# Performance work log

Hardware: AMD Instinct MI355X
Metric: run time of the kernel (lower is better)

Reference implementation:

```python
import jax, jax.numpy as jnp
import numpy as np

DIM = 2                 # spatial dimension (fixed to 2 in the source)
T = 6                   # number_of_time_points
DT = 1.0 / (T - 1)


def _mlp(z, W1, b1, W2, b2, W3, b3):
    # Linear_Tanh(4->10), Linear_Tanh(10->10), Linear(10->3)
    h = jnp.tanh(z @ W1 + b1)
    h = jnp.tanh(h @ W2 + b2)
    return h @ W3 + b3


def _sym_block(o):
    # o[...,3] -> symmetric 2x2 block: off-diag o[...,0], diag exp(o[...,1]), exp(o[...,2])
    off = o[..., 0]
    row0 = jnp.stack([jnp.exp(o[..., 1]), off], axis=-1)
    row1 = jnp.stack([off, jnp.exp(o[..., 2])], axis=-1)
    return jnp.stack([row0, row1], axis=-2)


def _kernel_blocks(x, y, params):
    # x: [b, nx, 2], y: [b, ny, 2] -> pairwise 2x2 kernel blocks [b, nx, ny, 2, 2]
    b, nx, _ = x.shape
    ny = y.shape[1]
    xx = jnp.broadcast_to(x[:, :, None, :], (b, nx, ny, DIM))
    yy = jnp.broadcast_to(y[:, None, :, :], (b, nx, ny, DIM))
    K1 = _sym_block(_mlp(jnp.concatenate([xx, yy], axis=-1), *params))
    K2 = _sym_block(_mlp(jnp.concatenate([yy, xx], axis=-1), *params))
    return 0.5 * (K1 + K2)


def _matvec(K, q):
    # block-matrix vector product: K [b,nx,ny,2,2] @ q [b,ny,2] -> [b,nx,2]
    return jnp.einsum('bxyij,byj->bxi', K, q)


def _forward(q_0, template_points, control_points, W1, b1, W2, b2, W3, b3):
    params = (W1, b1, W2, b2, W3, b3)
    bts = q_0.shape[0]
    p = jnp.broadcast_to(control_points[None], (bts,) + control_points.shape)
    p_t, q_t = [p], [q_0]

    def ham(pp, qq):
        dh_dq = _matvec(_kernel_blocks(pp, pp, params), qq)
        return 0.5 * jnp.sum(qq * dh_dq), dh_dq

    # Hamiltonian shooting: T steps of symplectic-Euler-like integration
    for _ in range(T):
        pc, qc = p_t[-1], q_t[-1]
        (_, dh_dq), dh_dp = jax.value_and_grad(ham, has_aux=True)(pc, qc)
        p_t.append(pc + DT * dh_dq)
        q_t.append(qc - DT * dh_dp)

    # flow the template points along the time-varying velocity field
    x = jnp.broadcast_to(template_points[None], (bts,) + template_points.shape)
    for pc, qc in zip(p_t, q_t):
        x = x + DT * _matvec(_kernel_blocks(x, pc, params), qc)
    return x


def setup_inputs() -> dict:
    key = jax.random.key(0)
    ks = jax.random.split(key, 8)
    bts, ncp, ntpl, H = 16, 64, 2048, 10
    # 8x8 control-point grid over [-2.5, 2.5]^2 (compute_grid with margin 0)
    ax = jnp.linspace(-2.5, 2.5, 8, dtype=jnp.float32)
    gx, gy = jnp.meshgrid(ax, ax, indexing='ij')
    control_points = jnp.stack([gx, gy], axis=-1).reshape(ncp, DIM)
    template_points = jax.random.normal(ks[0], (ntpl, DIM), dtype=jnp.float32)
    q_0 = 0.05 * jax.random.normal(ks[1], (bts, ncp, DIM), dtype=jnp.float32)
    W1 = 0.5 * jax.random.normal(ks[2], (2 * DIM, H), dtype=jnp.float32)
    b1 = jnp.zeros((H,), dtype=jnp.float32)
    W2 = 0.5 * jax.random.normal(ks[3], (H, H), dtype=jnp.float32)
    b2 = jnp.zeros((H,), dtype=jnp.float32)
    W3 = 0.5 * jax.random.normal(ks[4], (H, DIM * (DIM + 1) // 2), dtype=jnp.float32)
    b3 = jnp.zeros((DIM * (DIM + 1) // 2,), dtype=jnp.float32)
    return {'q_0': q_0, 'template_points': template_points, 'control_points': control_points,
            'W1': W1, 'b1': b1, 'W2': W2, 'b2': b2, 'W3': W3, 'b3': b3}


def reference(q_0, template_points, control_points, W1, b1, W2, b2, W3, b3):
    return _forward(q_0, template_points, control_points, W1, b1, W2, b2, W3, b3)
```

## Files before the change

kernel.cpp:

```cpp
#include <hip/hip_runtime.h>
#include <hip/hip_fp16.h>

#define NCP    64
#define BTS    16
#define NTPL   2048
#define TSTEPS 6
#define DTF    0.2f
#define L2E    1.4426950408889634f

__device__ __forceinline__ float fast_rcp(float x) { return __builtin_amdgcn_rcpf(x); }
__device__ __forceinline__ float fexp2(float x)    { return __builtin_amdgcn_exp2f(x); }
__device__ __forceinline__ float fast_tanh(float x) {
    float e = __expf(2.0f * x);
    return 1.0f - 2.0f * fast_rcp(1.0f + e);
}

__device__ __forceinline__ void load_raw_w(
    const float* __restrict__ W1, const float* __restrict__ b1,
    const float* __restrict__ W2, const float* __restrict__ W3,
    int lane, float (&w)[180])
{
    float cA = (lane < 40) ? W1[lane] : (lane < 50 ? b1[lane - 40] : 0.f);
    float cB0 = W2[lane];
    float cB1 = (lane < 36) ? W2[64 + lane] : 0.f;
    float cC  = (lane < 30) ? W3[lane] : 0.f;
#pragma unroll
    for (int t = 0; t < 50; ++t)  w[t] = __shfl(cA, t);
#pragma unroll
    for (int t = 0; t < 64; ++t)  w[50 + t] = __shfl(cB0, t);
#pragma unroll
    for (int t = 0; t < 36; ++t)  w[114 + t] = __shfl(cB1, t);
#pragma unroll
    for (int t = 0; t < 30; ++t)  w[150 + t] = __shfl(cC, t);
}

__device__ __forceinline__ void load_w_h2(const float* __restrict__ wt,
                                          int lane, __half2 (&wh)[180])
{
    float c0 = wt[lane];
    float c1 = wt[64 + lane];
    float c2 = wt[128 + lane];
#pragma unroll
    for (int t = 0; t < 180; ++t) {
        int src = (t < 150) ? t : (t + 10);
        int ch = src >> 6, ix = src & 63;
        float v = (ch == 0) ? c0 : (ch == 1) ? c1 : c2;
        wh[t] = __float2half2_rn(__shfl(v, ix));
    }
}

__device__ __forceinline__ void kblock4_h2(
    const float (&x0)[4], const float (&x1)[4], float p0, float p1,
    const __half2 (&wh)[180], const __half2 (&b2h)[10], const __half2 (&b3h)[3],
    float (&M00)[4], float (&M01)[4], float (&M11)[4])
{
    const __half2 one = __float2half2_rn(1.0f);

    __half2 Z0[4], Z1[4], Z2[4], Z3[4];
#pragma unroll
    for (int m = 0; m < 4; ++m) {
        Z0[m] = __floats2half2_rn(x0[m], p0);
        Z1[m] = __floats2half2_rn(x1[m], p1);
        Z2[m] = __lowhigh2highlow(Z0[m]);
        Z3[m] = __lowhigh2highlow(Z1[m]);
    }

    __half2 r[4][10];
#pragma unroll
    for (int k = 0; k < 10; ++k) {
        __half2 w0 = wh[k], w1 = wh[10 + k], w2 = wh[20 + k], w3 = wh[30 + k];
        __half2 bb = wh[40 + k];
#pragma unroll
        for (int m = 0; m < 4; ++m) {
            __half2 t = __hfma2(Z3[m], w3,
                        __hfma2(Z2[m], w2,
                        __hfma2(Z1[m], w1,
                        __hfma2(Z0[m], w0, bb))));
            r[m][k] = h2rcp(__hadd2(one, h2exp2(t)));
        }
    }

    __half2 u[4][10];
#pragma unroll
    for (int k = 0; k < 10; ++k) {
        __half2 ww = wh[50 + k];
        __half2 bb = b2h[k];
#pragma unroll
        for (int m = 0; m < 4; ++m) u[m][k] = __hfma2(r[m][0], ww, bb);
    }
#pragma unroll
    for (int c = 1; c < 10; ++c) {
#pragma unroll
        for (int k = 0; k < 10; ++k) {
            __half2 ww = wh[50 + c * 10 + k];
#pragma unroll
            for (int m = 0; m < 4; ++m) u[m][k] = __hfma2(r[m][c], ww, u[m][k]);
        }
    }

    __half2 O[4], A[4], B[4];
#pragma unroll
    for (int m = 0; m < 4; ++m) { O[m] = b3h[0]; A[m] = b3h[1]; B[m] = b3h[2]; }
#pragma unroll
    for (int c = 0; c < 10; ++c) {
        __half2 c0 = wh[150 + c], c1 = wh[160 + c], c2 = wh[170 + c];
#pragma unroll
        for (int m = 0; m < 4; ++m) {
            __half2 g = h2rcp(__hadd2(one, h2exp2(u[m][c])));
            O[m] = __hfma2(g, c0, O[m]);
            A[m] = __hfma2(g, c1, A[m]);
            B[m] = __hfma2(g, c2, B[m]);
        }
    }
#pragma unroll
    for (int m = 0; m < 4; ++m) {
        M00[m] = fexp2(__low2float(A[m])) + fexp2(__high2float(A[m]));
        M01[m] = __low2float(O[m]) + __high2float(O[m]);
        M11[m] = fexp2(__low2float(B[m])) + fexp2(__high2float(B[m]));
    }
}

__device__ __forceinline__ void kblock_s0(
    float x0, float x1, float p0, float p1,
    const float (&w)[180], const float (&b2t)[10], const float (&b3t)[3],
    float& M00, float& M01, float& M11)
{
    float ra[10], rb[10];
#pragma unroll
    for (int k = 0; k < 10; ++k) {
        float ta = fmaf(p1, w[30 + k],
                   fmaf(p0, w[20 + k],
                   fmaf(x1, w[10 + k],
                   fmaf(x0, w[k], w[40 + k]))));
        float tb = fmaf(x1, w[30 + k],
                   fmaf(x0, w[20 + k],
                   fmaf(p1, w[10 + k],
                   fmaf(p0, w[k], w[40 + k]))));
        ra[k] = fast_rcp(1.0f + fexp2(ta));
        rb[k] = fast_rcp(1.0f + fexp2(tb));
    }
    float ua[10], ub[10];
#pragma unroll
    for (int k = 0; k < 10; ++k) {
        float bb = b2t[k];
        ua[k] = fmaf(ra[0], w[50 + k], bb);
        ub[k] = fmaf(rb[0], w[50 + k], bb);
    }
#pragma unroll
    for (int c = 1; c < 10; ++c) {
#pragma unroll
        for (int k = 0; k < 10; ++k) {
            float ww = w[50 + c * 10 + k];
            ua[k] = fmaf(ra[c], ww, ua[k]);
            ub[k] = fmaf(rb[c], ww, ub[k]);
        }
    }
    float Oa = b3t[0], Ob = b3t[0];
    float T1a = b3t[1], T1b = b3t[1];
    float T2a = b3t[2], T2b = b3t[2];
#pragma unroll
    for (int c = 0; c < 10; ++c) {
        float r2a = fast_rcp(1.0f + fexp2(ua[c]));
        float r2b = fast_rcp(1.0f + fexp2(ub[c]));
        Oa  = fmaf(r2a, w[150 + c], Oa);   Ob  = fmaf(r2b, w[150 + c], Ob);
        T1a = fmaf(r2a, w[160 + c], T1a);  T1b = fmaf(r2b, w[160 + c], T1b);
        T2a = fmaf(r2a, w[170 + c], T2a);  T2b = fmaf(r2b, w[170 + c], T2b);
    }
    M00 = fexp2(T1a) + fexp2(T1b);
    M01 = Oa + Ob;
    M11 = fexp2(T2a) + fexp2(T2b);
}

__device__ __forceinline__ void shoot_body(
    int batch, int a, int b,
    float pax, float pay, float qax, float qay,
    float pbx, float pby, float qbx, float qby,
    const float (&w)[180],
    const float* __restrict__ b2, const float* __restrict__ b3,
    float* __restrict__ p_out, float* __restrict__ q_out)
{
    float dhq_x = 0.f, dhq_y = 0.f;
    float g_x = 0.f, g_y = 0.f;
    float cross = fmaf(qax, qby, qay * qbx);

#pragma unroll
    for (int e = 0; e < 2; ++e) {
        float z0 = e ? pbx : pax;
        float z1 = e ? pby : pay;
        float z2 = e ? pax : pbx;
        float z3 = e ? pay : pby;

        float h1[10];
#pragma unroll
        for (int k = 0; k < 10; ++k) {
            float u = fmaf(z3, w[30 + k],
                      fmaf(z2, w[20 + k],
                      fmaf(z1, w[10 + k],
                      fmaf(z0, w[k], w[40 + k]))));
            h1[k] = fast_tanh(u);
        }
        float u2[10];
#pragma unroll
        for (int k = 0; k < 10; ++k) u2[k] = b2[k];
#pragma unroll
        for (int c = 0; c < 10; ++c) {
#pragma unroll
            for (int k = 0; k < 10; ++k) u2[k] = fmaf(h1[c], w[50 + c * 10 + k], u2[k]);
        }
        float h2[10];
        float o0 = b3[0], o1 = b3[1], o2 = b3[2];
#pragma unroll
        for (int c = 0; c < 10; ++c) {
            h2[c] = fast_tanh(u2[c]);
            o0 = fmaf(h2[c], w[150 + c * 3 + 0], o0);
            o1 = fmaf(h2[c], w[150 + c * 3 + 1], o1);
            o2 = fmaf(h2[c], w[150 + c * 3 + 2], o2);
        }
        float e1 = __expf(o1), e2 = __expf(o2);

        dhq_x = fmaf(0.5f, fmaf(e1, qbx, o0 * qby), dhq_x);
        dhq_y = fmaf(0.5f, fmaf(o0, qbx, e2 * qby), dhq_y);

        float d0 = cross;
        float d1 = e1 * qax * qbx;
        float d2 = e2 * qay * qby;

        float du2[10];
#pragma unroll
        for (int c = 0; c < 10; ++c) {
            float dh2 = fmaf(w[150 + c * 3 + 0], d0,
                        fmaf(w[150 + c * 3 + 1], d1, w[150 + c * 3 + 2] * d2));
            du2[c] = dh2 * (1.0f - h2[c] * h2[c]);
        }
        float du1[10];
#pragma unroll
        for (int c = 0; c < 10; ++c) {
            float dh1 = 0.f;
#pragma unroll
            for (int k = 0; k < 10; ++k) dh1 = fmaf(w[50 + c * 10 + k], du2[k], dh1);
            du1[c] = dh1 * (1.0f - h1[c] * h1[c]);
        }
        int c0 = e ? 2 : 0;
        float ga = 0.f, gb = 0.f;
#pragma unroll
        for (int k = 0; k < 10; ++k) {
            ga = fmaf(w[(0 + c0) * 10 + k], du1[k], ga);
            gb = fmaf(w[(1 + c0) * 10 + k], du1[k], gb);
        }
        g_x = fmaf(0.5f, ga, g_x);
        g_y = fmaf(0.5f, gb, g_y);
    }

#pragma unroll
    for (int off = 32; off > 0; off >>= 1) {
        dhq_x += __shfl_xor(dhq_x, off);
        dhq_y += __shfl_xor(dhq_y, off);
        g_x   += __shfl_xor(g_x, off);
        g_y   += __shfl_xor(g_y, off);
    }

    if (b == 0) {
        float* pO = p_out + (batch * NCP + a) * 2;
        float* qO = q_out + (batch * NCP + a) * 2;
        pO[0] = fmaf(DTF, dhq_x, pax);
        pO[1] = fmaf(DTF, dhq_y, pay);
        qO[0] = fmaf(-DTF, g_x, qax);
        qO[1] = fmaf(-DTF, g_y, qay);
    }
}

__global__ __launch_bounds__(64, 1)
void shoot0_fused(const float* __restrict__ q0, const float* __restrict__ cp,
                  const float* __restrict__ tpl,
                  const float* __restrict__ W1, const float* __restrict__ b1,
                  const float* __restrict__ W2, const float* __restrict__ b2,
                  const float* __restrict__ W3, const float* __restrict__ b3,
                  float* __restrict__ p_hist, float* __restrict__ q_hist,
                  float* __restrict__ wt, float* __restrict__ out)
{
    int blk = blockIdx.x;
    int lane = threadIdx.x;

    if (blk < BTS * NCP) {
        float w[180];
        load_raw_w(W1, b1, W2, W3, lane, w);
        int batch = blk >> 6;
        int a = blk & (NCP - 1);
        int b = lane;
        float pax = cp[2 * a], pay = cp[2 * a + 1];
        float pbx = cp[2 * b], pby = cp[2 * b + 1];
        float qax = q0[(batch * NCP + a) * 2 + 0], qay = q0[(batch * NCP + a) * 2 + 1];
        float qbx = q0[(batch * NCP + b) * 2 + 0], qby = q0[(batch * NCP + b) * 2 + 1];
        shoot_body(batch, a, b, pax, pay, qax, qay, pbx, pby, qbx, qby,
                   w, b2, b3,
                   p_hist + (size_t)1 * BTS * NCP * 2,
                   q_hist + (size_t)1 * BTS * NCP * 2);
        return;
    }
    if (blk == BTS * NCP) {
        int t = lane;
        if (t < 40) wt[t] = 2.0f * L2E * W1[t];
        if (t < 10) wt[40 + t] = 2.0f * L2E * b1[t];
        for (int i = t; i < 100; i += 64) wt[50 + i] = -4.0f * L2E * W2[i];
        if (t < 10) {
            float s = b2[t];
            for (int c = 0; c < 10; ++c) s += W2[c * 10 + t];
            wt[150 + t] = 2.0f * L2E * s;
            wt[160 + t] = -W3[t * 3 + 0];
            wt[170 + t] = -2.0f * L2E * W3[t * 3 + 1];
            wt[180 + t] = -2.0f * L2E * W3[t * 3 + 2];
        }
        if (t < 3) {
            float s = b3[t];
            for (int c = 0; c < 10; ++c) s += W3[c * 3 + t];
            wt[190 + t] = (t == 0) ? 0.5f * s : fmaf(L2E, s, -1.0f);
        }
        return;
    }

    int i = blk - (BTS * NCP + 1);
    int j = lane;

    float w[180];
    load_raw_w(W1, b1, W2, W3, j, w);

    float b2t[10], b3t[3];
#pragma unroll
    for (int k = 0; k < 10; ++k) {
        float s = b2[k];
#pragma unroll
        for (int c = 0; c < 10; ++c) s += w[50 + c * 10 + k];
        b2t[k] = 2.0f * L2E * s;
    }
#pragma unroll
    for (int t = 0; t < 3; ++t) {
        float s = b3[t];
#pragma unroll
        for (int c = 0; c < 10; ++c) s += w[150 + c * 3 + t];
        b3t[t] = (t == 0) ? 0.5f * s : fmaf(L2E, s, -1.0f);
    }
#pragma unroll
    for (int t = 0; t < 50; ++t) w[t] *= 2.0f * L2E;
#pragma unroll
    for (int t = 50; t < 150; ++t) w[t] *= -4.0f * L2E;
    {
        float c0a[10], c1a[10], c2a[10];
#pragma unroll
        for (int k = 0; k < 10; ++k) {
            c0a[k] = -w[150 + 3 * k];
            c1a[k] = -2.0f * L2E * w[151 + 3 * k];
            c2a[k] = -2.0f * L2E * w[152 + 3 * k];
        }
#pragma unroll
        for (int k = 0; k < 10; ++k) {
            w[150 + k] = c0a[k];
            w[160 + k] = c1a[k];
            w[170 + k] = c2a[k];
        }
    }

    float x0 = tpl[2 * i], x1 = tpl[2 * i + 1];
    float p0 = cp[2 * j],  p1 = cp[2 * j + 1];

    float M00, M01, M11;
    kblock_s0(x0, x1, p0, p1, w, b2t, b3t, M00, M01, M11);

    const float2* __restrict__ q = (const float2*)q0;
#pragma unroll
    for (int bt = 0; bt < BTS; ++bt) {
        float2 qq = q[bt * NCP + j];
        float vx = fmaf(M00, qq.x, M01 * qq.y);
        float vy = fmaf(M01, qq.x, M11 * qq.y);
#pragma unroll
        for (int off = 32; off > 0; off >>= 1) {
            vx += __shfl_xor(vx, off);
            vy += __shfl_xor(vy, off);
        }
        if (j == 0) {
            out[((size_t)bt * NTPL + i) * 2 + 0] = fmaf(DTF, vx, x0);
            out[((size_t)bt * NTPL + i) * 2 + 1] = fmaf(DTF, vy, x1);
        }
    }
}

__global__ __launch_bounds__(64, 1)
void shoot_step(const float* __restrict__ p_in, const float* __restrict__ q_in,
                float* __restrict__ p_out, float* __restrict__ q_out,
                const float* __restrict__ W1, const float* __restrict__ b1,
                const float* __restrict__ W2, const float* __restrict__ b2,
                const float* __restrict__ W3, const float* __restrict__ b3)
{
    int blk = blockIdx.x;
    int batch = blk >> 6;
    int a = blk & (NCP - 1);
    int b = threadIdx.x;

    float w[180];
    load_raw_w(W1, b1, W2, W3, b, w);

    const float* pB = p_in + batch * NCP * 2;
    const float* qB = q_in + batch * NCP * 2;
    float pax = pB[a * 2 + 0], pay = pB[a * 2 + 1];
    float qax = qB[a * 2 + 0], qay = qB[a * 2 + 1];
    float pbx = pB[b * 2 + 0], pby = pB[b * 2 + 1];
    float qbx = qB[b * 2 + 0], qby = qB[b * 2 + 1];

    shoot_body(batch, a, b, pax, pay, qax, qay, pbx, pby, qbx, qby,
               w, b2, b3, p_out, q_out);
}

__global__ __launch_bounds__(256, 1)
void flow_rest(const float* __restrict__ p_hist, const float* __restrict__ q_hist,
               float* __restrict__ out, const float* __restrict__ wt)
{
    int wid = blockIdx.x * 4 + (threadIdx.x >> 6);
    int j = threadIdx.x & 63;
    int u0 = wid * 4;
    int batch = u0 >> 11;
    int i0 = u0 & (NTPL - 1);

    __half2 wh[180];
    load_w_h2(wt, j, wh);
    __half2 b2h[10], b3h[3];
#pragma unroll
    for (int k = 0; k < 10; ++k) b2h[k] = __float2half2_rn(wt[150 + k]);
#pragma unroll
    for (int t = 0; t < 3; ++t)  b3h[t] = __float2half2_rn(wt[190 + t]);

    const float2* __restrict__ ph = (const float2*)p_hist;
    const float2* __restrict__ qh = (const float2*)q_hist;

    size_t ob = ((size_t)batch * NTPL + i0) * 2;
    float x0[4], x1[4];
#pragma unroll
    for (int m = 0; m < 4; ++m) {
        x0[m] = out[ob + 2 * m];
        x1[m] = out[ob + 2 * m + 1];
    }

#pragma unroll
    for (int s = 0; s < TSTEPS; ++s) {
        int idx = ((s + 1) * BTS + batch) * NCP + j;
        float2 P = ph[idx];
        float2 Q = qh[idx];
        float M00[4], M01[4], M11[4];
        kblock4_h2(x0, x1, P.x, P.y, wh, b2h, b3h, M00, M01, M11);
        float vx[4], vy[4];
#pragma unroll
        for (int m = 0; m < 4; ++m) {
            vx[m] = fmaf(M00[m], Q.x, M01[m] * Q.y);
            vy[m] = fmaf(M01[m], Q.x, M11[m] * Q.y);
        }
#pragma unroll
        for (int off = 32; off > 0; off >>= 1) {
#pragma unroll
            for (int m = 0; m < 4; ++m) {
                vx[m] += __shfl_xor(vx[m], off);
                vy[m] += __shfl_xor(vy[m], off);
            }
        }
#pragma unroll
        for (int m = 0; m < 4; ++m) {
            x0[m] = fmaf(DTF, vx[m], x0[m]);
            x1[m] = fmaf(DTF, vy[m], x1[m]);
        }
    }

    if (j == 0) {
#pragma unroll
        for (int m = 0; m < 4; ++m) {
            out[ob + 2 * m]     = x0[m];
            out[ob + 2 * m + 1] = x1[m];
        }
    }
}

extern "C" void kernel_launch(void* const* d_in, const int* in_sizes, int n_in,
                              void* d_out, int out_size, void* d_ws, size_t ws_size,
                              hipStream_t stream)
{
    const float* q0  = (const float*)d_in[0];
    const float* tpl = (const float*)d_in[1];
    const float* cp  = (const float*)d_in[2];
    const float* W1  = (const float*)d_in[3];
    const float* b1  = (const float*)d_in[4];
    const float* W2  = (const float*)d_in[5];
    const float* b2  = (const float*)d_in[6];
    const float* W3  = (const float*)d_in[7];
    const float* b3  = (const float*)d_in[8];
    float* out = (float*)d_out;

    float* ws = (float*)d_ws;
    const int slab = BTS * NCP * 2;
    float* p_hist = ws;
    float* q_hist = ws + (size_t)7 * slab;
    float* wt     = ws + (size_t)14 * slab;

    shoot0_fused<<<BTS * NCP + 1 + NTPL, 64, 0, stream>>>(
        q0, cp, tpl, W1, b1, W2, b2, W3, b3, p_hist, q_hist, wt, out);

    for (int s = 1; s < TSTEPS; ++s) {
        shoot_step<<<BTS * NCP, 64, 0, stream>>>(
            p_hist + (size_t)s * slab, q_hist + (size_t)s * slab,
            p_hist + (size_t)(s + 1) * slab, q_hist + (size_t)(s + 1) * slab,
            W1, b1, W2, b2, W3, b3);
    }

    flow_rest<<<BTS * NTPL / 16, 256, 0, stream>>>(p_hist, q_hist, out, wt);
}
```

Baseline: 273.9 us.

## Fuse each template flow step into the matching shooting step launch

Replaces the single final flow kernel, which looped over all six time steps, with a combined kernel launched once per shooting step. Each launch runs both the next shooting step and the template-point flow update for the current step, plus a final flow-only launch. The aim is to overlap the small, low-occupancy shooting work with the flow work so the GPU stays busier. In exchange, flow blocks shrink from 256 to 64 threads and the template positions are re-read and re-written in global memory at every step, and weights are reloaded each launch.

New measurement: 329.5 us. 20.3% more time.

```diff
diff --git a/kernel.cpp b/kernel.cpp
--- a/kernel.cpp
+++ b/kernel.cpp
@@ -384,38 +384,37 @@
 }
 
 __global__ __launch_bounds__(64, 1)
-void shoot_step(const float* __restrict__ p_in, const float* __restrict__ q_in,
+void step_fused(const float* __restrict__ p_in, const float* __restrict__ q_in,
                 float* __restrict__ p_out, float* __restrict__ q_out,
                 const float* __restrict__ W1, const float* __restrict__ b1,
                 const float* __restrict__ W2, const float* __restrict__ b2,
-                const float* __restrict__ W3, const float* __restrict__ b3)
+                const float* __restrict__ W3, const float* __restrict__ b3,
+                const float* __restrict__ wt, float* __restrict__ out,
+                int with_shoot)
 {
     int blk = blockIdx.x;
-    int batch = blk >> 6;
-    int a = blk & (NCP - 1);
-    int b = threadIdx.x;
-
-    float w[180];
-    load_raw_w(W1, b1, W2, W3, b, w);
-
-    const float* pB = p_in + batch * NCP * 2;
-    const float* qB = q_in + batch * NCP * 2;
-    float pax = pB[a * 2 + 0], pay = pB[a * 2 + 1];
-    float qax = qB[a * 2 + 0], qay = qB[a * 2 + 1];
-    float pbx = pB[b * 2 + 0], pby = pB[b * 2 + 1];
-    float qbx = qB[b * 2 + 0], qby = qB[b * 2 + 1];
-
-    shoot_body(batch, a, b, pax, pay, qax, qay, pbx, pby, qbx, qby,
-               w, b2, b3, p_out, q_out);
-}
-
-__global__ __launch_bounds__(256, 1)
-void flow_rest(const float* __restrict__ p_hist, const float* __restrict__ q_hist,
-               float* __restrict__ out, const float* __restrict__ wt)
-{
-    int wid = blockIdx.x * 4 + (threadIdx.x >> 6);
-    int j = threadIdx.x & 63;
-    int u0 = wid * 4;
+    int lane = threadIdx.x;
+
+    if (with_shoot && blk < BTS * NCP) {
+        float w[180];
+        load_raw_w(W1, b1, W2, W3, lane, w);
+        int batch = blk >> 6;
+        int a = blk & (NCP - 1);
+        int b = lane;
+        const float* pB = p_in + batch * NCP * 2;
+        const float* qB = q_in + batch * NCP * 2;
+        float pax = pB[a * 2 + 0], pay = pB[a * 2 + 1];
+        float qax = qB[a * 2 + 0], qay = qB[a * 2 + 1];
+        float pbx = pB[b * 2 + 0], pby = pB[b * 2 + 1];
+        float qbx = qB[b * 2 + 0], qby = qB[b * 2 + 1];
+        shoot_body(batch, a, b, pax, pay, qax, qay, pbx, pby, qbx, qby,
+                   w, b2, b3, p_out, q_out);
+        return;
+    }
+
+    int flk = with_shoot ? (blk - BTS * NCP) : blk;
+    int j = lane;
+    int u0 = flk * 4;
     int batch = u0 >> 11;
     int i0 = u0 & (NTPL - 1);
 
@@ -427,8 +426,11 @@
 #pragma unroll
     for (int t = 0; t < 3; ++t)  b3h[t] = __float2half2_rn(wt[190 + t]);
 
-    const float2* __restrict__ ph = (const float2*)p_hist;
-    const float2* __restrict__ qh = (const float2*)q_hist;
+    const float2* __restrict__ ph = (const float2*)p_in;
+    const float2* __restrict__ qh = (const float2*)q_in;
+    int idx = batch * NCP + j;
+    float2 P = ph[idx];
+    float2 Q = qh[idx];
 
     size_t ob = ((size_t)batch * NTPL + i0) * 2;
     float x0[4], x1[4];
@@ -438,39 +440,27 @@
         x1[m] = out[ob + 2 * m + 1];
     }
 
-#pragma unroll
-    for (int s = 0; s < TSTEPS; ++s) {
-        int idx = ((s + 1) * BTS + batch) * NCP + j;
-        float2 P = ph[idx];
-        float2 Q = qh[idx];
-        float M00[4], M01[4], M11[4];
-        kblock4_h2(x0, x1, P.x, P.y, wh, b2h, b3h, M00, M01, M11);
-        float vx[4], vy[4];
+    float M00[4], M01[4], M11[4];
+    kblock4_h2(x0, x1, P.x, P.y, wh, b2h, b3h, M00, M01, M11);
+    float vx[4], vy[4];
+#pragma unroll
+    for (int m = 0; m < 4; ++m) {
+        vx[m] = fmaf(M00[m], Q.x, M01[m] * Q.y);
+        vy[m] = fmaf(M01[m], Q.x, M11[m] * Q.y);
+    }
+#pragma unroll
+    for (int off = 32; off > 0; off >>= 1) {
 #pragma unroll
         for (int m = 0; m < 4; ++m) {
-            vx[m] = fmaf(M00[m], Q.x, M01[m] * Q.y);
-            vy[m] = fmaf(M01[m], Q.x, M11[m] * Q.y);
-        }
-#pragma unroll
-        for (int off = 32; off > 0; off >>= 1) {
-#pragma unroll
-            for (int m = 0; m < 4; ++m) {
-                vx[m] += __shfl_xor(vx[m], off);
-                vy[m] += __shfl_xor(vy[m], off);
-            }
-        }
+            vx[m] += __shfl_xor(vx[m], off);
+            vy[m] += __shfl_xor(vy[m], off);
+        }
+    }
+    if (j == 0) {
 #pragma unroll
         for (int m = 0; m < 4; ++m) {
-            x0[m] = fmaf(DTF, vx[m], x0[m]);
-            x1[m] = fmaf(DTF, vy[m], x1[m]);
-        }
-    }
-
-    if (j == 0) {
-#pragma unroll
-        for (int m = 0; m < 4; ++m) {
-            out[ob + 2 * m]     = x0[m];
-            out[ob + 2 * m + 1] = x1[m];
+            out[ob + 2 * m]     = fmaf(DTF, vx[m], x0[m]);
+            out[ob + 2 * m + 1] = fmaf(DTF, vy[m], x1[m]);
         }
     }
 }
@@ -496,15 +486,20 @@
     float* q_hist = ws + (size_t)7 * slab;
     float* wt     = ws + (size_t)14 * slab;
 
+    const int NFLOWBLK = BTS * NTPL / 4;
+
     shoot0_fused<<<BTS * NCP + 1 + NTPL, 64, 0, stream>>>(
         q0, cp, tpl, W1, b1, W2, b2, W3, b3, p_hist, q_hist, wt, out);
 
-    for (int s = 1; s < TSTEPS; ++s) {
-        shoot_step<<<BTS * NCP, 64, 0, stream>>>(
-            p_hist + (size_t)s * slab, q_hist + (size_t)s * slab,
-            p_hist + (size_t)(s + 1) * slab, q_hist + (size_t)(s + 1) * slab,
-            W1, b1, W2, b2, W3, b3);
-    }
-
-    flow_rest<<<BTS * NTPL / 16, 256, 0, stream>>>(p_hist, q_hist, out, wt);
-}
+    for (int k = 1; k < TSTEPS; ++k) {
+        step_fused<<<BTS * NCP + NFLOWBLK, 64, 0, stream>>>(
+            p_hist + (size_t)k * slab, q_hist + (size_t)k * slab,
+            p_hist + (size_t)(k + 1) * slab, q_hist + (size_t)(k + 1) * slab,
+            W1, b1, W2, b2, W3, b3, wt, out, 1);
+    }
+
+    step_fused<<<NFLOWBLK, 64, 0, stream>>>(
+        p_hist + (size_t)TSTEPS * slab, q_hist + (size_t)TSTEPS * slab,
+        nullptr, nullptr,
+        W1, b1, W2, b2, W3, b3, wt, out, 0);
+}
```
